# Kernel optimization log

Measured on AMD Instinct MI355X. Metric: run time of the kernel, lower is better.

Reference implementation:

```python
import jax, jax.numpy as jnp
import numpy as np

TOP_K = 4
SWIGLU_LIMIT = 7.0
SWIGLU_ALPHA = 1.702
RMS_EPS = 1e-5

H = 768      # hidden_size
I = 768      # intermediate_size
E = 128      # num_experts
B = 32       # tokens


def setup_inputs() -> dict:
    key = jax.random.key(0)
    ks = jax.random.split(key, 6)
    scale = 0.02
    return {
        "x": jax.random.normal(ks[0], (B, H), dtype=jnp.float32),
        "norm_scale": jnp.ones((H,), dtype=jnp.float32),
        "gate_w": jax.random.normal(ks[1], (H, E), dtype=jnp.float32) * scale,
        "mlp1_w": jax.random.normal(ks[2], (E, 2 * I, H), dtype=jnp.float32) * scale,
        "mlp1_b": jax.random.normal(ks[3], (E, 2 * I), dtype=jnp.float32) * scale,
        "mlp2_w": jax.random.normal(ks[4], (E, H, I), dtype=jnp.float32) * scale,
        "mlp2_b": jax.random.normal(ks[5], (E, H), dtype=jnp.float32) * scale,
    }


def _rmsnorm(x, scale):
    var = jnp.mean(jnp.square(x), axis=-1, keepdims=True)
    return x * jax.lax.rsqrt(var + RMS_EPS) * scale


def _swiglu(x, alpha=SWIGLU_ALPHA, limit=SWIGLU_LIMIT):
    x_glu, x_linear = x[..., ::2], x[..., 1::2]
    x_glu = jnp.minimum(x_glu, limit)
    x_linear = jnp.clip(x_linear, -limit, limit)
    out_glu = x_glu * jax.nn.sigmoid(alpha * x_glu)
    return out_glu * (x_linear + 1)


def reference(x, norm_scale, gate_w, mlp1_w, mlp1_b, mlp2_w, mlp2_b):
    t = _rmsnorm(x, norm_scale)                      # [B, H]
    g = t @ gate_w                                   # [B, E]
    expert_weights, expert_indices = jax.lax.top_k(g, k=TOP_K)
    expert_weights = jax.nn.softmax(expert_weights, axis=-1)  # [B, k]

    w1 = mlp1_w[expert_indices]                      # [B, k, 2I, H]
    b1 = mlp1_b[expert_indices]                      # [B, k, 2I]
    h = jnp.einsum('beck,bk->bec', w1, t) + b1       # [B, k, 2I]
    h = _swiglu(h)                                   # [B, k, I]

    w2 = mlp2_w[expert_indices]                      # [B, k, H, I]
    b2 = mlp2_b[expert_indices]                      # [B, k, H]
    o = jnp.einsum('beck,bek->bec', w2, h) + b2      # [B, k, H]
    o = jnp.einsum('bec,be->bc', o, expert_weights)  # [B, H]
    return x + o
```

## Files before the change

kernel.cpp:

```cpp
#include <hip/hip_runtime.h>
#include <math.h>

#define Hdim 768
#define I2   1536
#define Idim 768
#define Edim 128
#define Bdim 32
#define TOPK 4
#define CHUNK 4
#define PARTS1 96
#define PARTS2 48

typedef float nvec4 __attribute__((ext_vector_type(4)));
__device__ __forceinline__ float4 NT4(const float4* p) {
    nvec4 v = __builtin_nontemporal_load((const nvec4*)p);
    return make_float4(v.x, v.y, v.z, v.w);
}

__global__ __launch_bounds__(256) void k_prep(
    const float* __restrict__ x, const float* __restrict__ ns,
    const float* __restrict__ gw, float* __restrict__ t_ws,
    int* __restrict__ combo, float* __restrict__ out) {
    __shared__ __align__(16) float t_lds[Hdim];
    __shared__ float red_s[4];
    __shared__ __align__(16) float4 acc_s[4][32];
    __shared__ __align__(16) float gval[Edim];
    __shared__ int   sel_s[TOPK];
    __shared__ float w_s[TOPK];
    const int b    = blockIdx.x;
    const int tid  = threadIdx.x;
    const int w    = tid >> 6;
    const int lane = tid & 63;
    const float* xr = x + b * Hdim;

    float ss = 0.f;
    for (int i = tid; i < Hdim; i += 256) { float v = xr[i]; ss += v * v; }
#pragma unroll
    for (int off = 1; off < 64; off <<= 1) ss += __shfl_xor(ss, off, 64);
    if (lane == 0) red_s[w] = ss;
    __syncthreads();
    const float rs = rsqrtf((red_s[0] + red_s[1] + red_s[2] + red_s[3]) / (float)Hdim + 1e-5f);
    for (int i = tid; i < Hdim; i += 256) {
        float xv = xr[i];
        float tv = xv * rs * ns[i];
        t_lds[i] = tv;
        t_ws[b * Hdim + i] = tv;
        out[b * Hdim + i] = xv;
    }
    __syncthreads();

    const int g = tid & 31;
    const int s = tid >> 5;
    const float* gwp = gw + (size_t)(s * 96) * Edim + 4 * g;
    float4 a = {0.f, 0.f, 0.f, 0.f};
#pragma unroll 8
    for (int h = 0; h < 96; ++h) {
        float tv = t_lds[s * 96 + h];
        float4 wv = *(const float4*)(gwp + (size_t)h * Edim);
        a.x += tv * wv.x; a.y += tv * wv.y;
        a.z += tv * wv.z; a.w += tv * wv.w;
    }
    a.x += __shfl_xor(a.x, 32, 64); a.y += __shfl_xor(a.y, 32, 64);
    a.z += __shfl_xor(a.z, 32, 64); a.w += __shfl_xor(a.w, 32, 64);
    if (lane < 32) acc_s[w][lane] = a;
    __syncthreads();

    if (w == 0) {
        if (lane < 32) {
            float4 s0 = acc_s[0][lane], s1 = acc_s[1][lane], s2 = acc_s[2][lane], s3 = acc_s[3][lane];
            float4 t4 = {s0.x + s1.x + s2.x + s3.x, s0.y + s1.y + s2.y + s3.y,
                         s0.z + s1.z + s2.z + s3.z, s0.w + s1.w + s2.w + s3.w};
            *(float4*)&gval[4 * lane] = t4;
        }
        float g0 = gval[lane], g1 = gval[lane + 64];
        bool p0 = false, p1 = false;
        float topv[TOPK]; int topi[TOPK];
#pragma unroll
        for (int k = 0; k < TOPK; ++k) {
            float c0 = p0 ? -3.0e38f : g0;
            float c1 = p1 ? -3.0e38f : g1;
            float v = fmaxf(c0, c1);
#pragma unroll
            for (int off = 1; off < 64; off <<= 1) v = fmaxf(v, __shfl_xor(v, off, 64));
            int cand = (c0 == v) ? lane : ((c1 == v) ? lane + 64 : 0x7fffffff);
#pragma unroll
            for (int off = 1; off < 64; off <<= 1) cand = min(cand, __shfl_xor(cand, off, 64));
            if (cand == lane) p0 = true;
            if (cand == lane + 64) p1 = true;
            topv[k] = v; topi[k] = cand;
        }
        if (lane == 0) {
            float m = topv[0], ex[TOPK], sum = 0.f;
#pragma unroll
            for (int k = 0; k < TOPK; ++k) { ex[k] = __expf(topv[k] - m); sum += ex[k]; }
            float inv = 1.0f / sum;
#pragma unroll
            for (int k = 0; k < TOPK; ++k) { sel_s[k] = topi[k]; w_s[k] = ex[k] * inv; }
        }
    }
    __syncthreads();
    if (tid < Edim) {
        int rv = 0;
#pragma unroll
        for (int k = 0; k < TOPK; ++k)
            if (sel_s[k] == tid)
                rv = (int)((__float_as_uint(w_s[k]) & ~3u) | (unsigned)k);
        combo[tid * Bdim + b] = rv;
    }
}

__global__ __launch_bounds__(256, 4) void k_mlp1(
    const float* __restrict__ w1, const float* __restrict__ b1,
    const float* __restrict__ t_ws, const int* __restrict__ combo,
    float* __restrict__ h_ws) {
    const int e    = blockIdx.x / PARTS1;
    const int part = blockIdx.x % PARTS1;
    __shared__ float4 t_lds[CHUNK][Hdim / 4];
    __shared__ float  b1_lds[16];
    __shared__ int    pair_s[Bdim];
    __shared__ int    cnt_s;
    const int tid  = threadIdx.x;
    const int wave = tid >> 6, lane = tid & 63;

    if (tid < 64) {
        int rv = (lane < Bdim) ? combo[e * Bdim + lane] : 0;
        float wv = __uint_as_float((unsigned)rv & ~3u);
        unsigned long long m = __ballot(wv > 0.f);
        if (wv > 0.f) {
            int idx = __popcll(m & ((1ull << lane) - 1ull));
            pair_s[idx] = lane * TOPK + (rv & 3);
        }
        if (lane == 0) cnt_s = (int)__popcll(m);
    }
    __syncthreads();
    const int count = cnt_s;
    if (count == 0) return;

    const int jbase = part * (Idim / PARTS1);
    const float* w1e = w1 + (size_t)e * I2 * Hdim;
    if (tid < 16) b1_lds[tid] = b1[e * I2 + 2 * jbase + tid];

    for (int i0 = 0; i0 < count; i0 += CHUNK) {
        const int nt = min(CHUNK, count - i0);
        __syncthreads();
        for (int i = 0; i < nt; ++i) {
            const float4* src = (const float4*)(t_ws + (size_t)(pair_s[i0 + i] >> 2) * Hdim);
            if (tid < Hdim / 4) t_lds[i][tid] = src[tid];
        }
        __syncthreads();
#pragma unroll
        for (int r = 0; r < 2; ++r) {
            const int j = jbase + wave * 2 + r;
            const float4* rg = (const float4*)(w1e + (size_t)(2 * j) * Hdim);
            const float4* rl = (const float4*)(w1e + (size_t)(2 * j + 1) * Hdim);
            float4 g0 = NT4(rg + lane), g1 = NT4(rg + lane + 64), g2 = NT4(rg + lane + 128);
            float4 l0 = NT4(rl + lane), l1 = NT4(rl + lane + 64), l2 = NT4(rl + lane + 128);
            float ag[CHUNK], al[CHUNK];
#pragma unroll
            for (int i = 0; i < CHUNK; ++i) {
                ag[i] = 0.f; al[i] = 0.f;
                if (i < nt) {
                    float4 t0 = t_lds[i][lane], t1 = t_lds[i][lane + 64], t2 = t_lds[i][lane + 128];
                    ag[i] = g0.x*t0.x + g0.y*t0.y + g0.z*t0.z + g0.w*t0.w
                          + g1.x*t1.x + g1.y*t1.y + g1.z*t1.z + g1.w*t1.w
                          + g2.x*t2.x + g2.y*t2.y + g2.z*t2.z + g2.w*t2.w;
                    al[i] = l0.x*t0.x + l0.y*t0.y + l0.z*t0.z + l0.w*t0.w
                          + l1.x*t1.x + l1.y*t1.y + l1.z*t1.z + l1.w*t1.w
                          + l2.x*t2.x + l2.y*t2.y + l2.z*t2.z + l2.w*t2.w;
                }
            }
            const float bg = b1_lds[2 * (wave * 2 + r)];
            const float bl = b1_lds[2 * (wave * 2 + r) + 1];
#pragma unroll
            for (int i = 0; i < CHUNK; ++i) {
                if (i < nt) {
                    const int odd = lane & 1;
                    float send = odd ? ag[i] : al[i];
                    float recv = __shfl_xor(send, 1, 64);
                    float v = (odd ? al[i] : ag[i]) + recv;
#pragma unroll
                    for (int off = 2; off < 64; off <<= 1) v += __shfl_xor(v, off, 64);
                    float vo = __shfl_xor(v, 1, 64);
                    float vg = odd ? vo : v;
                    float vl = odd ? v : vo;
                    float glu = fminf(vg + bg, 7.0f);
                    float lin = fminf(fmaxf(vl + bl, -7.0f), 7.0f);
                    float og = glu / (1.0f + __expf(-1.702f * glu));
                    if (lane == 0)
                        h_ws[(size_t)pair_s[i0 + i] * Idim + j] = og * (lin + 1.0f);
                }
            }
        }
    }
}

__global__ __launch_bounds__(256, 4) void k_mlp2(
    const float* __restrict__ w2, const float* __restrict__ b2,
    const float* __restrict__ h_ws, const int* __restrict__ combo,
    float* __restrict__ out) {
    const int e    = blockIdx.x / PARTS2;
    const int part = blockIdx.x % PARTS2;
    __shared__ float4 h_lds[CHUNK][Idim / 4];
    __shared__ float  b2_lds[16];
    __shared__ int    pair_s[Bdim];
    __shared__ float  wt_s[Bdim];
    __shared__ int    cnt_s;
    const int tid  = threadIdx.x;
    const int wave = tid >> 6, lane = tid & 63;

    if (tid < 64) {
        int rv = (lane < Bdim) ? combo[e * Bdim + lane] : 0;
        float wv = __uint_as_float((unsigned)rv & ~3u);
        unsigned long long m = __ballot(wv > 0.f);
        if (wv > 0.f) {
            int idx = __popcll(m & ((1ull << lane) - 1ull));
            pair_s[idx] = lane * TOPK + (rv & 3);
            wt_s[idx]   = wv;
        }
        if (lane == 0) cnt_s = (int)__popcll(m);
    }
    __syncthreads();
    const int count = cnt_s;
    if (count == 0) return;

    const int cbase = part * (Hdim / PARTS2);
    const float* w2e = w2 + (size_t)e * Hdim * Idim;
    if (tid < 16) b2_lds[tid] = b2[e * Hdim + cbase + tid];

    for (int i0 = 0; i0 < count; i0 += CHUNK) {
        const int nt = min(CHUNK, count - i0);
        __syncthreads();
        for (int i = 0; i < nt; ++i) {
            const float4* src = (const float4*)(h_ws + (size_t)pair_s[i0 + i] * Idim);
            if (tid < Idim / 4) h_lds[i][tid] = src[tid];
        }
        __syncthreads();
#pragma unroll
        for (int rp = 0; rp < 2; ++rp) {
            const int c0 = cbase + wave * 4 + 2 * rp;
            const float4* r0 = (const float4*)(w2e + (size_t)c0 * Idim);
            const float4* r1 = (const float4*)(w2e + (size_t)(c0 + 1) * Idim);
            float4 a0 = NT4(r0 + lane), a1 = NT4(r0 + lane + 64), a2 = NT4(r0 + lane + 128);
            float4 d0 = NT4(r1 + lane), d1 = NT4(r1 + lane + 64), d2 = NT4(r1 + lane + 128);
            float ao0[CHUNK], ao1[CHUNK];
#pragma unroll
            for (int i = 0; i < CHUNK; ++i) {
                ao0[i] = 0.f; ao1[i] = 0.f;
                if (i < nt) {
                    float4 h0 = h_lds[i][lane], h1 = h_lds[i][lane + 64], h2 = h_lds[i][lane + 128];
                    ao0[i] = a0.x*h0.x + a0.y*h0.y + a0.z*h0.z + a0.w*h0.w
                           + a1.x*h1.x + a1.y*h1.y + a1.z*h1.z + a1.w*h1.w
                           + a2.x*h2.x + a2.y*h2.y + a2.z*h2.z + a2.w*h2.w;
                    ao1[i] = d0.x*h0.x + d0.y*h0.y + d0.z*h0.z + d0.w*h0.w
                           + d1.x*h1.x + d1.y*h1.y + d1.z*h1.z + d1.w*h1.w
                           + d2.x*h2.x + d2.y*h2.y + d2.z*h2.z + d2.w*h2.w;
                }
            }
#pragma unroll
            for (int i = 0; i < CHUNK; ++i) {
                if (i < nt) {
                    const int odd = lane & 1;
                    float send = odd ? ao0[i] : ao1[i];
                    float recv = __shfl_xor(send, 1, 64);
                    float v = (odd ? ao1[i] : ao0[i]) + recv;
#pragma unroll
                    for (int off = 2; off < 64; off <<= 1) v += __shfl_xor(v, off, 64);
                    const int c = c0 + odd;
                    if (lane < 2)
                        atomicAdd(&out[(size_t)(pair_s[i0 + i] >> 2) * Hdim + c],
                                  (v + b2_lds[c - cbase]) * wt_s[i0 + i]);
                }
            }
        }
    }
}

extern "C" void kernel_launch(void* const* d_in, const int* in_sizes, int n_in,
                              void* d_out, int out_size, void* d_ws, size_t ws_size,
                              hipStream_t stream) {
    const float* x  = (const float*)d_in[0];
    const float* ns = (const float*)d_in[1];
    const float* gw = (const float*)d_in[2];
    const float* w1 = (const float*)d_in[3];
    const float* b1 = (const float*)d_in[4];
    const float* w2 = (const float*)d_in[5];
    const float* b2 = (const float*)d_in[6];
    float* out = (float*)d_out;
    float* ws  = (float*)d_ws;

    float* t_ws  = ws;
    int*   combo = (int*)(ws + 24576);
    float* h_ws  = ws + 28672;

    k_prep<<<Bdim, 256, 0, stream>>>(x, ns, gw, t_ws, combo, out);
    k_mlp1<<<Edim * PARTS1, 256, 0, stream>>>(w1, b1, t_ws, combo, h_ws);
    k_mlp2<<<Edim * PARTS2, 256, 0, stream>>>(w2, b2, h_ws, combo, out);
}
```

Measured before the change: 104.9 us.

## Fuse routing prep into MLP1 kernel with global flag spin-wait

Merges the prep kernel (rmsnorm, gating, top-k) into the MLP1 kernel. The first 32 blocks compute the routing, and the remaining blocks spin on a global atomic counter before reading the routing data. The intent is to remove one kernel launch boundary and let the MLP1 blocks get scheduled early. In exchange it adds a memset launch and relaxed-atomic spin-waiting. Since the spinning blocks issue no weight loads before the flag, the weight streaming itself is not overlapped with prep. The relaxed ordering also leaves some risk around memory visibility.

```diff
diff --git a/kernel.cpp b/kernel.cpp
--- a/kernel.cpp
+++ b/kernel.cpp
@@ -10,6 +10,7 @@
 #define CHUNK 4
 #define PARTS1 96
 #define PARTS2 48
+#define NBP  32
 
 typedef float nvec4 __attribute__((ext_vector_type(4)));
 __device__ __forceinline__ float4 NT4(const float4* p) {
@@ -17,110 +18,125 @@
     return make_float4(v.x, v.y, v.z, v.w);
 }
 
-__global__ __launch_bounds__(256) void k_prep(
+__global__ __launch_bounds__(256, 4) void k_prep_mlp1(
     const float* __restrict__ x, const float* __restrict__ ns,
-    const float* __restrict__ gw, float* __restrict__ t_ws,
-    int* __restrict__ combo, float* __restrict__ out) {
+    const float* __restrict__ gw,
+    const float* __restrict__ w1, const float* __restrict__ b1,
+    float* __restrict__ t_ws, int* __restrict__ combo,
+    float* __restrict__ h_ws, float* __restrict__ out,
+    int* __restrict__ flag) {
     __shared__ __align__(16) float t_lds[Hdim];
     __shared__ float red_s[4];
     __shared__ __align__(16) float4 acc_s[4][32];
     __shared__ __align__(16) float gval[Edim];
     __shared__ int   sel_s[TOPK];
     __shared__ float w_s[TOPK];
-    const int b    = blockIdx.x;
+    __shared__ float4 stage[CHUNK][Hdim / 4];
+    __shared__ float  b1_lds[16];
+    __shared__ int    pair_s[Bdim];
+    __shared__ int    cnt_s;
+
+    const int bid  = blockIdx.x;
     const int tid  = threadIdx.x;
     const int w    = tid >> 6;
     const int lane = tid & 63;
-    const float* xr = x + b * Hdim;
-
-    float ss = 0.f;
-    for (int i = tid; i < Hdim; i += 256) { float v = xr[i]; ss += v * v; }
-#pragma unroll
-    for (int off = 1; off < 64; off <<= 1) ss += __shfl_xor(ss, off, 64);
-    if (lane == 0) red_s[w] = ss;
+
+    if (bid < NBP) {
+        const int b = bid;
+        const float* xr = x + b * Hdim;
+
+        float ss = 0.f;
+        for (int i = tid; i < Hdim; i += 256) { float v = xr[i]; ss += v * v; }
+#pragma unroll
+        for (int off = 1; off < 64; off <<= 1) ss += __shfl_xor(ss, off, 64);
+        if (lane == 0) red_s[w] = ss;
+        __syncthreads();
+        const float rs = rsqrtf((red_s[0] + red_s[1] + red_s[2] + red_s[3]) / (float)Hdim + 1e-5f);
+        for (int i = tid; i < Hdim; i += 256) {
+            float xv = xr[i];
+            float tv = xv * rs * ns[i];
+            t_lds[i] = tv;
+            __hip_atomic_store(&t_ws[b * Hdim + i], tv,
+                               __ATOMIC_RELAXED, __HIP_MEMORY_SCOPE_AGENT);
+            out[b * Hdim + i] = xv;
+        }
+        __syncthreads();
+
+        const int g = tid & 31;
+        const int s = tid >> 5;
+        const float* gwp = gw + (size_t)(s * 96) * Edim + 4 * g;
+        float4 a = {0.f, 0.f, 0.f, 0.f};
+#pragma unroll 8
+        for (int h = 0; h < 96; ++h) {
+            float tv = t_lds[s * 96 + h];
+            float4 wv = *(const float4*)(gwp + (size_t)h * Edim);
+            a.x += tv * wv.x; a.y += tv * wv.y;
+            a.z += tv * wv.z; a.w += tv * wv.w;
+        }
+        a.x += __shfl_xor(a.x, 32, 64); a.y += __shfl_xor(a.y, 32, 64);
+        a.z += __shfl_xor(a.z, 32, 64); a.w += __shfl_xor(a.w, 32, 64);
+        if (lane < 32) acc_s[w][lane] = a;
+        __syncthreads();
+
+        if (w == 0) {
+            if (lane < 32) {
+                float4 s0 = acc_s[0][lane], s1 = acc_s[1][lane], s2 = acc_s[2][lane], s3 = acc_s[3][lane];
+                float4 t4 = {s0.x + s1.x + s2.x + s3.x, s0.y + s1.y + s2.y + s3.y,
+                             s0.z + s1.z + s2.z + s3.z, s0.w + s1.w + s2.w + s3.w};
+                *(float4*)&gval[4 * lane] = t4;
+            }
+            float g0 = gval[lane], g1 = gval[lane + 64];
+            bool p0 = false, p1 = false;
+            float topv[TOPK]; int topi[TOPK];
+#pragma unroll
+            for (int k = 0; k < TOPK; ++k) {
+                float c0 = p0 ? -3.0e38f : g0;
+                float c1 = p1 ? -3.0e38f : g1;
+                float v = fmaxf(c0, c1);
+#pragma unroll
+                for (int off = 1; off < 64; off <<= 1) v = fmaxf(v, __shfl_xor(v, off, 64));
+                int cand = (c0 == v) ? lane : ((c1 == v) ? lane + 64 : 0x7fffffff);
+#pragma unroll
+                for (int off = 1; off < 64; off <<= 1) cand = min(cand, __shfl_xor(cand, off, 64));
+                if (cand == lane) p0 = true;
+                if (cand == lane + 64) p1 = true;
+                topv[k] = v; topi[k] = cand;
+            }
+            if (lane == 0) {
+                float m = topv[0], ex[TOPK], sum = 0.f;
+#pragma unroll
+                for (int k = 0; k < TOPK; ++k) { ex[k] = __expf(topv[k] - m); sum += ex[k]; }
+                float inv = 1.0f / sum;
+#pragma unroll
+                for (int k = 0; k < TOPK; ++k) { sel_s[k] = topi[k]; w_s[k] = ex[k] * inv; }
+            }
+        }
+        __syncthreads();
+        if (tid < Edim) {
+            int rv = 0;
+#pragma unroll
+            for (int k = 0; k < TOPK; ++k)
+                if (sel_s[k] == tid)
+                    rv = (int)((__float_as_uint(w_s[k]) & ~3u) | (unsigned)k);
+            __hip_atomic_store(&combo[tid * Bdim + b], rv,
+                               __ATOMIC_RELAXED, __HIP_MEMORY_SCOPE_AGENT);
+        }
+        asm volatile("s_waitcnt vmcnt(0)" ::: "memory");
+        __syncthreads();
+        if (tid == 0)
+            __hip_atomic_fetch_add(flag, 1, __ATOMIC_RELAXED, __HIP_MEMORY_SCOPE_AGENT);
+        return;
+    }
+
+    const int e    = (bid - NBP) / PARTS1;
+    const int part = (bid - NBP) % PARTS1;
+    const int wave = w;
+
+    if (tid == 0) {
+        while (__hip_atomic_load(flag, __ATOMIC_RELAXED, __HIP_MEMORY_SCOPE_AGENT) < NBP)
+            __builtin_amdgcn_s_sleep(16);
+    }
     __syncthreads();
-    const float rs = rsqrtf((red_s[0] + red_s[1] + red_s[2] + red_s[3]) / (float)Hdim + 1e-5f);
-    for (int i = tid; i < Hdim; i += 256) {
-        float xv = xr[i];
-        float tv = xv * rs * ns[i];
-        t_lds[i] = tv;
-        t_ws[b * Hdim + i] = tv;
-        out[b * Hdim + i] = xv;
-    }
-    __syncthreads();
-
-    const int g = tid & 31;
-    const int s = tid >> 5;
-    const float* gwp = gw + (size_t)(s * 96) * Edim + 4 * g;
-    float4 a = {0.f, 0.f, 0.f, 0.f};
-#pragma unroll 8
-    for (int h = 0; h < 96; ++h) {
-        float tv = t_lds[s * 96 + h];
-        float4 wv = *(const float4*)(gwp + (size_t)h * Edim);
-        a.x += tv * wv.x; a.y += tv * wv.y;
-        a.z += tv * wv.z; a.w += tv * wv.w;
-    }
-    a.x += __shfl_xor(a.x, 32, 64); a.y += __shfl_xor(a.y, 32, 64);
-    a.z += __shfl_xor(a.z, 32, 64); a.w += __shfl_xor(a.w, 32, 64);
-    if (lane < 32) acc_s[w][lane] = a;
-    __syncthreads();
-
-    if (w == 0) {
-        if (lane < 32) {
-            float4 s0 = acc_s[0][lane], s1 = acc_s[1][lane], s2 = acc_s[2][lane], s3 = acc_s[3][lane];
-            float4 t4 = {s0.x + s1.x + s2.x + s3.x, s0.y + s1.y + s2.y + s3.y,
-                         s0.z + s1.z + s2.z + s3.z, s0.w + s1.w + s2.w + s3.w};
-            *(float4*)&gval[4 * lane] = t4;
-        }
-        float g0 = gval[lane], g1 = gval[lane + 64];
-        bool p0 = false, p1 = false;
-        float topv[TOPK]; int topi[TOPK];
-#pragma unroll
-        for (int k = 0; k < TOPK; ++k) {
-            float c0 = p0 ? -3.0e38f : g0;
-            float c1 = p1 ? -3.0e38f : g1;
-            float v = fmaxf(c0, c1);
-#pragma unroll
-            for (int off = 1; off < 64; off <<= 1) v = fmaxf(v, __shfl_xor(v, off, 64));
-            int cand = (c0 == v) ? lane : ((c1 == v) ? lane + 64 : 0x7fffffff);
-#pragma unroll
-            for (int off = 1; off < 64; off <<= 1) cand = min(cand, __shfl_xor(cand, off, 64));
-            if (cand == lane) p0 = true;
-            if (cand == lane + 64) p1 = true;
-            topv[k] = v; topi[k] = cand;
-        }
-        if (lane == 0) {
-            float m = topv[0], ex[TOPK], sum = 0.f;
-#pragma unroll
-            for (int k = 0; k < TOPK; ++k) { ex[k] = __expf(topv[k] - m); sum += ex[k]; }
-            float inv = 1.0f / sum;
-#pragma unroll
-            for (int k = 0; k < TOPK; ++k) { sel_s[k] = topi[k]; w_s[k] = ex[k] * inv; }
-        }
-    }
-    __syncthreads();
-    if (tid < Edim) {
-        int rv = 0;
-#pragma unroll
-        for (int k = 0; k < TOPK; ++k)
-            if (sel_s[k] == tid)
-                rv = (int)((__float_as_uint(w_s[k]) & ~3u) | (unsigned)k);
-        combo[tid * Bdim + b] = rv;
-    }
-}
-
-__global__ __launch_bounds__(256, 4) void k_mlp1(
-    const float* __restrict__ w1, const float* __restrict__ b1,
-    const float* __restrict__ t_ws, const int* __restrict__ combo,
-    float* __restrict__ h_ws) {
-    const int e    = blockIdx.x / PARTS1;
-    const int part = blockIdx.x % PARTS1;
-    __shared__ float4 t_lds[CHUNK][Hdim / 4];
-    __shared__ float  b1_lds[16];
-    __shared__ int    pair_s[Bdim];
-    __shared__ int    cnt_s;
-    const int tid  = threadIdx.x;
-    const int wave = tid >> 6, lane = tid & 63;
 
     if (tid < 64) {
         int rv = (lane < Bdim) ? combo[e * Bdim + lane] : 0;
@@ -145,7 +161,7 @@
         __syncthreads();
         for (int i = 0; i < nt; ++i) {
             const float4* src = (const float4*)(t_ws + (size_t)(pair_s[i0 + i] >> 2) * Hdim);
-            if (tid < Hdim / 4) t_lds[i][tid] = src[tid];
+            if (tid < Hdim / 4) stage[i][tid] = src[tid];
         }
         __syncthreads();
 #pragma unroll
@@ -160,7 +176,7 @@
             for (int i = 0; i < CHUNK; ++i) {
                 ag[i] = 0.f; al[i] = 0.f;
                 if (i < nt) {
-                    float4 t0 = t_lds[i][lane], t1 = t_lds[i][lane + 64], t2 = t_lds[i][lane + 128];
+                    float4 t0 = stage[i][lane], t1 = stage[i][lane + 64], t2 = stage[i][lane + 128];
                     ag[i] = g0.x*t0.x + g0.y*t0.y + g0.z*t0.z + g0.w*t0.w
                           + g1.x*t1.x + g1.y*t1.y + g1.z*t1.z + g1.w*t1.w
                           + g2.x*t2.x + g2.y*t2.y + g2.z*t2.z + g2.w*t2.w;
@@ -291,8 +307,10 @@
     float* t_ws  = ws;
     int*   combo = (int*)(ws + 24576);
     float* h_ws  = ws + 28672;
-
-    k_prep<<<Bdim, 256, 0, stream>>>(x, ns, gw, t_ws, combo, out);
-    k_mlp1<<<Edim * PARTS1, 256, 0, stream>>>(w1, b1, t_ws, combo, h_ws);
+    int*   flag  = (int*)(ws + 126976);
+
+    hipMemsetAsync(flag, 0, sizeof(int), stream);
+    k_prep_mlp1<<<NBP + Edim * PARTS1, 256, 0, stream>>>(
+        x, ns, gw, w1, b1, t_ws, combo, h_ws, out, flag);
     k_mlp2<<<Edim * PARTS2, 256, 0, stream>>>(w2, b2, h_ws, combo, out);
 }
```

After: 113.2 us. +7.9%, slower.
